# Optimization experiments

Hardware: AMD Instinct MI355X
Metric: run time of the kernel (lower is better)

The kernel has to match this reference:

```python
import math
import jax, jax.numpy as jnp
import numpy as np

B, H, S, D = 2, 16, 2048, 1024
DK = D // H  # 64


def setup_inputs() -> dict:
    key = jax.random.key(0)
    k1, k2, k3, k4, k5 = jax.random.split(key, 5)
    scale = np.float32(0.02)
    return {
        "x": jax.random.normal(k1, (B, H, S, D), dtype=jnp.float32),
        "wq": jax.random.normal(k2, (DK, D), dtype=jnp.float32) * scale,
        "wk": jax.random.normal(k3, (DK, D), dtype=jnp.float32) * scale,
        "wv": jax.random.normal(k4, (DK, D), dtype=jnp.float32) * scale,
        "wo": jax.random.normal(k5, (D, D), dtype=jnp.float32) * scale,
    }


def reference(x, wq, wk, wv, wo):
    # x: [B, H, S, D]; wq/wk/wv: [dk, D]; wo: [D, D]
    b, h, s, d = x.shape
    xq = jnp.einsum("bhsd,kd->bhsk", x, wq)  # [B,H,S,dk]
    xk = jnp.einsum("bhsd,kd->bhsk", x, wk)
    xv = jnp.einsum("bhsd,kd->bhsk", x, wv)
    # NOTE: original scales by sqrt(hidden_dim), not sqrt(dk)
    inv_scale = np.float32(1.0 / math.sqrt(d))
    score = jnp.einsum("bhsk,bhtk->bhst", xq, xk) * inv_scale  # [B,H,S,S]
    attn = jax.nn.softmax(score, axis=-1).astype(xq.dtype)
    out = jnp.einsum("bhst,bhtk->bhsk", attn, xv)  # [B,H,S,dk]
    out = out.transpose(0, 2, 1, 3).reshape(b, s, h * (wq.shape[0]))  # [B,S,H*dk]
    return out @ wo.T  # [B,S,D]
```

## Files before the change

### kernel.cpp

```cpp
#include <hip/hip_runtime.h>
#include <math.h>

#define BB 2
#define HH 16
#define SS 2048
#define DD 1024
#define DK 64
#define BHS (BB*HH*SS)
#define QSCALE 0.04508422f

typedef short  bf16x8  __attribute__((ext_vector_type(8)));
typedef float  floatx4 __attribute__((ext_vector_type(4)));
typedef unsigned short u16;

#define MFMA(a,b,c) __builtin_amdgcn_mfma_f32_16x16x32_bf16((a),(b),(c),0,0,0)

__device__ __forceinline__ unsigned cvt_pk_bf16(float lo, float hi) {
    unsigned r;
    asm("v_cvt_pk_bf16_f32 %0, %1, %2" : "=v"(r) : "v"(lo), "v"(hi));
    return r;
}
__device__ __forceinline__ bf16x8 ldfrag(const u16* p) {
    union { uint4 u; bf16x8 b; } c;
    c.u = *(const uint4*)p;
    return c.b;
}
__device__ __forceinline__ void stbf4(u16* p, float4 t) {
    union { unsigned u[2]; uint2 v; } c;
    c.u[0] = cvt_pk_bf16(t.x, t.y);
    c.u[1] = cvt_pk_bf16(t.z, t.w);
    *(uint2*)p = c.v;
}
__device__ __forceinline__ void st4s(u16* p, float a, float b, float c, float d) {
    unsigned x = cvt_pk_bf16(a, b), y = cvt_pk_bf16(c, d);
    p[0]  = (u16)x; p[16] = (u16)(x >> 16);
    p[32] = (u16)y; p[48] = (u16)(y >> 16);
}

#define WQKV_CHUNKS (192*1024/4)
#define WO_CHUNKS   (1024*1024/4)
__global__ __launch_bounds__(256) void convert_w(
    const float* __restrict__ wq, const float* __restrict__ wk,
    const float* __restrict__ wv, const float* __restrict__ wo,
    u16* __restrict__ wqkv, u16* __restrict__ wo_bf)
{
    int i = blockIdx.x * 256 + threadIdx.x;
    if (i < WQKV_CHUNKS) {
        int r = i >> 8;
        int c = i & 255;
        const float* src = (r < 64) ? wq : ((r < 128) ? wk : wv);
        float4 t = *(const float4*)(src + (size_t)(r & 63) * DD + c * 4);
        stbf4(wqkv + (size_t)r * DD + c * 4, t);
    } else if (i < WQKV_CHUNKS + WO_CHUNKS) {
        int j = i - WQKV_CHUNKS;
        float4 t = *(const float4*)(wo + (size_t)j * 4);
        stbf4(wo_bf + (size_t)j * 4, t);
    }
}

__global__ __launch_bounds__(256) void qkv_proj(
    const float* __restrict__ x, const u16* __restrict__ wqkv,
    u16* __restrict__ q, u16* __restrict__ k, u16* __restrict__ vT)
{
    __shared__ __align__(16) u16 Xs[64][72];
    __shared__ __align__(16) u16 Ws[192][72];
    const int tid  = threadIdx.x;
    const int w    = tid >> 6;
    const int lane = tid & 63;
    const int quad = lane >> 4;
    const int l16  = lane & 15;
    const int rowbase = blockIdx.x * 64;

    floatx4 acc[12];
#pragma unroll
    for (int n = 0; n < 12; ++n) acc[n] = (floatx4){0.f,0.f,0.f,0.f};

    for (int k0 = 0; k0 < DD; k0 += 64) {
#pragma unroll
        for (int it = 0; it < 4; ++it) {
            int li = tid + it * 256;
            int r  = li >> 4;
            int c4 = li & 15;
            float4 t = *(const float4*)(x + (size_t)(rowbase + r) * DD + k0 + c4 * 4);
            stbf4(&Xs[r][c4 * 4], t);
        }
#pragma unroll
        for (int it = 0; it < 6; ++it) {
            int li = tid + it * 256;
            int r  = li >> 3;
            int c8 = li & 7;
            *(uint4*)&Ws[r][c8 * 8] =
                *(const uint4*)(wqkv + (size_t)r * DD + k0 + c8 * 8);
        }
        __syncthreads();

        bf16x8 a0 = ldfrag(&Xs[w * 16 + l16][quad * 8]);
        bf16x8 a1 = ldfrag(&Xs[w * 16 + l16][32 + quad * 8]);
#pragma unroll
        for (int n = 0; n < 12; ++n) {
            bf16x8 b0 = ldfrag(&Ws[n * 16 + l16][quad * 8]);
            bf16x8 b1 = ldfrag(&Ws[n * 16 + l16][32 + quad * 8]);
            acc[n] = MFMA(a0, b0, acc[n]);
            acc[n] = MFMA(a1, b1, acc[n]);
        }
        __syncthreads();
    }

#pragma unroll
    for (int r = 0; r < 4; ++r) {
        int row = w * 16 + quad * 4 + r;
        size_t m = (size_t)(rowbase + row);
        st4s(&q[m * DK + l16], acc[0][r] * QSCALE, acc[1][r] * QSCALE,
                               acc[2][r] * QSCALE, acc[3][r] * QSCALE);
        st4s(&k[m * DK + l16], acc[4][r], acc[5][r], acc[6][r], acc[7][r]);
    }
    u16 (*Vbuf)[72] = Xs;
#pragma unroll
    for (int r = 0; r < 4; ++r) {
        int row = w * 16 + quad * 4 + r;
        st4s(&Vbuf[row][l16], acc[8][r], acc[9][r], acc[10][r], acc[11][r]);
    }
    __syncthreads();
    {
        const int dk = tid >> 2;
        const int sc = (tid & 3) * 16;
        const int bh = rowbase >> 11;
        const int s0 = rowbase & 2047;
        union { u16 s[16]; uint4 u[2]; } t;
#pragma unroll
        for (int u = 0; u < 16; ++u) t.s[u] = Vbuf[sc + u][dk];
        uint4* dst = (uint4*)(vT + ((size_t)(bh * DK + dk)) * SS + s0 + sc);
        dst[0] = t.u[0];
        dst[1] = t.u[1];
    }
}

__global__ __launch_bounds__(256) void flash_attn(
    const u16* __restrict__ q, const u16* __restrict__ k,
    const u16* __restrict__ vT, u16* __restrict__ ao)
{
    __shared__ __align__(16) u16 Qs[64][72];
    __shared__ __align__(16) u16 Ks[64][72];
    __shared__ __align__(16) u16 Vt[64][72];
    __shared__ __align__(16) u16 Ps[4][16][72];
    const int tid  = threadIdx.x;
    const int w    = tid >> 6;
    const int lane = tid & 63;
    const int quad = lane >> 4;
    const int l16  = lane & 15;
    const int qt   = blockIdx.x;
    const int bh   = blockIdx.y;
    const size_t kbase = (size_t)bh * SS * DK;
    const size_t vbase = (size_t)bh * DK * SS;

#pragma unroll
    for (int it = 0; it < 2; ++it) {
        int li = tid + it * 256;
        int r  = li >> 3;
        int c8 = li & 7;
        *(uint4*)&Qs[r][c8 * 8] =
            *(const uint4*)(q + kbase + (size_t)(qt * 64 + r) * DK + c8 * 8);
    }

    float m_i[4], l_i[4];
    floatx4 acc_o[4];
#pragma unroll
    for (int r = 0; r < 4; ++r) { m_i[r] = -INFINITY; l_i[r] = 0.f; }
#pragma unroll
    for (int n = 0; n < 4; ++n) acc_o[n] = (floatx4){0.f,0.f,0.f,0.f};
    __syncthreads();

    for (int kt = 0; kt < SS / 64; ++kt) {
#pragma unroll
        for (int it = 0; it < 2; ++it) {
            int li = tid + it * 256;
            int r  = li >> 3;
            int c8 = li & 7;
            *(uint4*)&Ks[r][c8 * 8] =
                *(const uint4*)(k + kbase + (size_t)(kt * 64 + r) * DK + c8 * 8);
            *(uint4*)&Vt[r][c8 * 8] =
                *(const uint4*)(vT + vbase + (size_t)r * SS + kt * 64 + c8 * 8);
        }
        __syncthreads();

        floatx4 sc[4];
        __builtin_amdgcn_s_setprio(1);
        {
            bf16x8 a0 = ldfrag(&Qs[w * 16 + l16][quad * 8]);
            bf16x8 a1 = ldfrag(&Qs[w * 16 + l16][32 + quad * 8]);
#pragma unroll
            for (int n = 0; n < 4; ++n) {
                sc[n] = (floatx4){0.f,0.f,0.f,0.f};
                bf16x8 b0 = ldfrag(&Ks[n * 16 + l16][quad * 8]);
                bf16x8 b1 = ldfrag(&Ks[n * 16 + l16][32 + quad * 8]);
                sc[n] = MFMA(a0, b0, sc[n]);
                sc[n] = MFMA(a1, b1, sc[n]);
            }
        }
        __builtin_amdgcn_s_setprio(0);

        float rmx[4];
#pragma unroll
        for (int r = 0; r < 4; ++r) {
            float rm = fmaxf(fmaxf(sc[0][r], sc[1][r]), fmaxf(sc[2][r], sc[3][r]));
#pragma unroll
            for (int off = 1; off < 16; off <<= 1)
                rm = fmaxf(rm, __shfl_xor(rm, off, 64));
            rmx[r] = rm;
        }
        int ok = (rmx[0] <= m_i[0] + 8.f) & (rmx[1] <= m_i[1] + 8.f) &
                 (rmx[2] <= m_i[2] + 8.f) & (rmx[3] <= m_i[3] + 8.f);
        if (!__all(ok)) {
#pragma unroll
            for (int r = 0; r < 4; ++r) {
                float mnew  = fmaxf(m_i[r], rmx[r]);
                float alpha = __builtin_amdgcn_exp2f(m_i[r] - mnew);
#pragma unroll
                for (int n = 0; n < 4; ++n) acc_o[n][r] *= alpha;
                l_i[r] *= alpha;
                m_i[r]  = mnew;
            }
        }
#pragma unroll
        for (int r = 0; r < 4; ++r) {
            float mi = m_i[r];
            float p0 = __builtin_amdgcn_exp2f(sc[0][r] - mi);
            float p1 = __builtin_amdgcn_exp2f(sc[1][r] - mi);
            float p2 = __builtin_amdgcn_exp2f(sc[2][r] - mi);
            float p3 = __builtin_amdgcn_exp2f(sc[3][r] - mi);
            float rs = (p0 + p1) + (p2 + p3);
#pragma unroll
            for (int off = 1; off < 16; off <<= 1)
                rs += __shfl_xor(rs, off, 64);
            l_i[r] += rs;
            st4s(&Ps[w][quad * 4 + r][l16], p0, p1, p2, p3);
        }

        __builtin_amdgcn_s_setprio(1);
#pragma unroll
        for (int kc = 0; kc < 2; ++kc) {
            bf16x8 a = ldfrag(&Ps[w][l16][kc * 32 + quad * 8]);
#pragma unroll
            for (int n = 0; n < 4; ++n) {
                bf16x8 b = ldfrag(&Vt[n * 16 + l16][kc * 32 + quad * 8]);
                acc_o[n] = MFMA(a, b, acc_o[n]);
            }
        }
        __builtin_amdgcn_s_setprio(0);
        __syncthreads();
    }

    const int b = bh >> 4, h = bh & 15;
#pragma unroll
    for (int r = 0; r < 4; ++r) {
        int srow = qt * 64 + w * 16 + quad * 4 + r;
        float rl = __builtin_amdgcn_rcpf(l_i[r]);
        size_t base = ((size_t)(b * SS + srow)) * (HH * DK) + h * 64;
        st4s(&ao[base + l16], acc_o[0][r] * rl, acc_o[1][r] * rl,
                              acc_o[2][r] * rl, acc_o[3][r] * rl);
    }
}

__global__ __launch_bounds__(256) void out_proj(
    const u16* __restrict__ ao, const u16* __restrict__ wo_bf,
    float* __restrict__ out)
{
    __shared__ __align__(16) u16 As[64][72];
    __shared__ __align__(16) u16 Bs[64][72];
    const int tid  = threadIdx.x;
    const int w    = tid >> 6;
    const int lane = tid & 63;
    const int quad = lane >> 4;
    const int l16  = lane & 15;
    const int mt = blockIdx.y;
    const int nt = blockIdx.x;

    floatx4 acc[4];
#pragma unroll
    for (int n = 0; n < 4; ++n) acc[n] = (floatx4){0.f,0.f,0.f,0.f};

    for (int k0 = 0; k0 < DD; k0 += 64) {
#pragma unroll
        for (int it = 0; it < 2; ++it) {
            int li = tid + it * 256;
            int r  = li >> 3;
            int c8 = li & 7;
            *(uint4*)&As[r][c8 * 8] =
                *(const uint4*)(ao + (size_t)(mt * 64 + r) * DD + k0 + c8 * 8);
            *(uint4*)&Bs[r][c8 * 8] =
                *(const uint4*)(wo_bf + (size_t)(nt * 64 + r) * DD + k0 + c8 * 8);
        }
        __syncthreads();

        bf16x8 a0 = ldfrag(&As[w * 16 + l16][quad * 8]);
        bf16x8 a1 = ldfrag(&As[w * 16 + l16][32 + quad * 8]);
#pragma unroll
        for (int n = 0; n < 4; ++n) {
            bf16x8 b0 = ldfrag(&Bs[n * 16 + l16][quad * 8]);
            bf16x8 b1 = ldfrag(&Bs[n * 16 + l16][32 + quad * 8]);
            acc[n] = MFMA(a0, b0, acc[n]);
            acc[n] = MFMA(a1, b1, acc[n]);
        }
        __syncthreads();
    }

#pragma unroll
    for (int r = 0; r < 4; ++r) {
        int row = mt * 64 + w * 16 + quad * 4 + r;
#pragma unroll
        for (int n = 0; n < 4; ++n)
            out[(size_t)row * DD + nt * 64 + n * 16 + l16] = acc[n][r];
    }
}

extern "C" void kernel_launch(void* const* d_in, const int* in_sizes, int n_in,
                              void* d_out, int out_size, void* d_ws, size_t ws_size,
                              hipStream_t stream) {
    const float* x  = (const float*)d_in[0];
    const float* wq = (const float*)d_in[1];
    const float* wk = (const float*)d_in[2];
    const float* wv = (const float*)d_in[3];
    const float* wo = (const float*)d_in[4];
    float* out = (float*)d_out;

    u16* q    = (u16*)d_ws;
    u16* k    = q    + (size_t)BHS * DK;
    u16* vT   = k    + (size_t)BHS * DK;
    u16* ao   = vT   + (size_t)BHS * DK;
    u16* wqkv = ao   + (size_t)BHS * DK;
    u16* wo_bf = wqkv + (size_t)192 * DD;

    convert_w<<<dim3((WQKV_CHUNKS + WO_CHUNKS) / 256), dim3(256), 0, stream>>>(
        wq, wk, wv, wo, wqkv, wo_bf);
    qkv_proj<<<dim3(BHS / 64), dim3(256), 0, stream>>>(x, wqkv, q, k, vT);
    flash_attn<<<dim3(SS / 64, BB * HH), dim3(256), 0, stream>>>(q, k, vT, ao);
    out_proj<<<dim3(DD / 64, (BB * SS) / 64), dim3(256), 0, stream>>>(ao, wo_bf, out);
}
```

Baseline: 574.6 us.

## Add register prefetch pipelining to all GEMM kernels and enlarge out_proj tiles

All three compute kernels now load the next K/V or weight tile into registers while computing on the current LDS tile, then store it to LDS between barriers, so global latency overlaps with MFMA work. qkv_proj moves to 512 threads split over row tiles and output-column groups, staging x in 256-wide chunks. out_proj grows from 64x64 to 128x128 tiles with 2x8 accumulators per wave for more operand reuse. The changes add register pressure and an extra barrier per iteration, and they set occupancy hints through launch_bounds.

After: 687.1 us. +19.6%, slower.

```diff
diff --git a/kernel.cpp b/kernel.cpp
--- a/kernel.cpp
+++ b/kernel.cpp
@@ -35,6 +35,10 @@
     unsigned x = cvt_pk_bf16(a, b), y = cvt_pk_bf16(c, d);
     p[0]  = (u16)x; p[16] = (u16)(x >> 16);
     p[32] = (u16)y; p[48] = (u16)(y >> 16);
+}
+__device__ __forceinline__ void st2s(u16* p, float a, float b) {
+    unsigned x = cvt_pk_bf16(a, b);
+    p[0]  = (u16)x; p[16] = (u16)(x >> 16);
 }
 
 #define WQKV_CHUNKS (192*1024/4)
@@ -58,84 +62,117 @@
     }
 }
 
-__global__ __launch_bounds__(256) void qkv_proj(
+__global__ __launch_bounds__(512, 4) void qkv_proj(
     const float* __restrict__ x, const u16* __restrict__ wqkv,
     u16* __restrict__ q, u16* __restrict__ k, u16* __restrict__ vT)
 {
-    __shared__ __align__(16) u16 Xs[64][72];
+    __shared__ __align__(16) u16 Xs[64][264];
     __shared__ __align__(16) u16 Ws[192][72];
     const int tid  = threadIdx.x;
     const int w    = tid >> 6;
     const int lane = tid & 63;
     const int quad = lane >> 4;
     const int l16  = lane & 15;
+    const int rt   = w & 3;
+    const int g    = w >> 2;
     const int rowbase = blockIdx.x * 64;
-
-    floatx4 acc[12];
-#pragma unroll
-    for (int n = 0; n < 12; ++n) acc[n] = (floatx4){0.f,0.f,0.f,0.f};
-
-    for (int k0 = 0; k0 < DD; k0 += 64) {
-#pragma unroll
-        for (int it = 0; it < 4; ++it) {
-            int li = tid + it * 256;
-            int r  = li >> 4;
-            int c4 = li & 15;
-            float4 t = *(const float4*)(x + (size_t)(rowbase + r) * DD + k0 + c4 * 4);
-            stbf4(&Xs[r][c4 * 4], t);
-        }
-#pragma unroll
-        for (int it = 0; it < 6; ++it) {
-            int li = tid + it * 256;
-            int r  = li >> 3;
-            int c8 = li & 7;
-            *(uint4*)&Ws[r][c8 * 8] =
-                *(const uint4*)(wqkv + (size_t)r * DD + k0 + c8 * 8);
-        }
-        __syncthreads();
-
-        bf16x8 a0 = ldfrag(&Xs[w * 16 + l16][quad * 8]);
-        bf16x8 a1 = ldfrag(&Xs[w * 16 + l16][32 + quad * 8]);
-#pragma unroll
-        for (int n = 0; n < 12; ++n) {
-            bf16x8 b0 = ldfrag(&Ws[n * 16 + l16][quad * 8]);
-            bf16x8 b1 = ldfrag(&Ws[n * 16 + l16][32 + quad * 8]);
-            acc[n] = MFMA(a0, b0, acc[n]);
-            acc[n] = MFMA(a1, b1, acc[n]);
-        }
-        __syncthreads();
-    }
-
-#pragma unroll
-    for (int r = 0; r < 4; ++r) {
-        int row = w * 16 + quad * 4 + r;
-        size_t m = (size_t)(rowbase + row);
-        st4s(&q[m * DK + l16], acc[0][r] * QSCALE, acc[1][r] * QSCALE,
-                               acc[2][r] * QSCALE, acc[3][r] * QSCALE);
-        st4s(&k[m * DK + l16], acc[4][r], acc[5][r], acc[6][r], acc[7][r]);
-    }
-    u16 (*Vbuf)[72] = Xs;
-#pragma unroll
-    for (int r = 0; r < 4; ++r) {
-        int row = w * 16 + quad * 4 + r;
-        st4s(&Vbuf[row][l16], acc[8][r], acc[9][r], acc[10][r], acc[11][r]);
+    const float* xb = x + (size_t)rowbase * DD;
+
+    float4 xreg[8];
+    uint4  wreg[3];
+
+    auto xload = [&](int qd) {
+#pragma unroll
+        for (int it = 0; it < 8; ++it) {
+            int li = tid + it * 512;
+            int r  = li >> 6, c4 = li & 63;
+            xreg[it] = *(const float4*)(xb + (size_t)r * DD + qd * 256 + c4 * 4);
+        }
+    };
+    auto xstore = [&]() {
+#pragma unroll
+        for (int it = 0; it < 8; ++it) {
+            int li = tid + it * 512;
+            int r  = li >> 6, c4 = li & 63;
+            stbf4(&Xs[r][c4 * 4], xreg[it]);
+        }
+    };
+    auto wload = [&](int kk) {
+#pragma unroll
+        for (int it = 0; it < 3; ++it) {
+            int li = tid + it * 512;
+            int r  = li >> 3, c8 = li & 7;
+            wreg[it] = *(const uint4*)(wqkv + (size_t)r * DD + kk * 64 + c8 * 8);
+        }
+    };
+    auto wstore = [&]() {
+#pragma unroll
+        for (int it = 0; it < 3; ++it) {
+            int li = tid + it * 512;
+            int r  = li >> 3, c8 = li & 7;
+            *(uint4*)&Ws[r][c8 * 8] = wreg[it];
+        }
+    };
+
+    floatx4 acc[6];
+#pragma unroll
+    for (int j = 0; j < 6; ++j) acc[j] = (floatx4){0.f,0.f,0.f,0.f};
+
+    xload(0); xstore();
+    wload(0); wstore();
+    __syncthreads();
+
+    for (int qd = 0; qd < 4; ++qd) {
+        if (qd < 3) xload(qd + 1);
+#pragma unroll
+        for (int ks = 0; ks < 4; ++ks) {
+            int kk = qd * 4 + ks;
+            if (kk < 15) wload(kk + 1);
+            bf16x8 a0 = ldfrag(&Xs[rt * 16 + l16][ks * 64 + quad * 8]);
+            bf16x8 a1 = ldfrag(&Xs[rt * 16 + l16][ks * 64 + 32 + quad * 8]);
+#pragma unroll
+            for (int j = 0; j < 6; ++j) {
+                int n = g * 6 + j;
+                bf16x8 b0 = ldfrag(&Ws[n * 16 + l16][quad * 8]);
+                bf16x8 b1 = ldfrag(&Ws[n * 16 + l16][32 + quad * 8]);
+                acc[j] = MFMA(a0, b0, acc[j]);
+                acc[j] = MFMA(a1, b1, acc[j]);
+            }
+            __syncthreads();
+            if (kk < 15) wstore();
+            if (ks == 3 && qd < 3) xstore();
+            __syncthreads();
+        }
+    }
+
+#pragma unroll
+    for (int rr = 0; rr < 4; ++rr) {
+        int rloc = rt * 16 + quad * 4 + rr;
+        size_t m = (size_t)(rowbase + rloc);
+        if (g == 0) {
+            st4s(&q[m * DK + l16], acc[0][rr] * QSCALE, acc[1][rr] * QSCALE,
+                                   acc[2][rr] * QSCALE, acc[3][rr] * QSCALE);
+            st2s(&k[m * DK + l16], acc[4][rr], acc[5][rr]);
+        } else {
+            st2s(&k[m * DK + 32 + l16], acc[0][rr], acc[1][rr]);
+            st4s(&Xs[rloc][l16], acc[2][rr], acc[3][rr],
+                                 acc[4][rr], acc[5][rr]);
+        }
     }
     __syncthreads();
     {
-        const int dk = tid >> 2;
-        const int sc = (tid & 3) * 16;
+        const int dk = tid >> 3;
+        const int sc = (tid & 7) * 8;
         const int bh = rowbase >> 11;
         const int s0 = rowbase & 2047;
-        union { u16 s[16]; uint4 u[2]; } t;
-#pragma unroll
-        for (int u = 0; u < 16; ++u) t.s[u] = Vbuf[sc + u][dk];
-        uint4* dst = (uint4*)(vT + ((size_t)(bh * DK + dk)) * SS + s0 + sc);
-        dst[0] = t.u[0];
-        dst[1] = t.u[1];
-    }
-}
-
-__global__ __launch_bounds__(256) void flash_attn(
+        union { u16 s[8]; uint4 u; } t;
+#pragma unroll
+        for (int u = 0; u < 8; ++u) t.s[u] = Xs[sc + u][dk];
+        *(uint4*)(vT + ((size_t)(bh * DK + dk)) * SS + s0 + sc) = t.u;
+    }
+}
+
+__global__ __launch_bounds__(256, 4) void flash_attn(
     const u16* __restrict__ q, const u16* __restrict__ k,
     const u16* __restrict__ vT, u16* __restrict__ ao)
 {
@@ -153,11 +190,30 @@
     const size_t kbase = (size_t)bh * SS * DK;
     const size_t vbase = (size_t)bh * DK * SS;
 
+    uint4 kreg[2], vreg[2];
+    auto kvload = [&](int kt) {
+#pragma unroll
+        for (int it = 0; it < 2; ++it) {
+            int li = tid + it * 256;
+            int r  = li >> 3, c8 = li & 7;
+            kreg[it] = *(const uint4*)(k + kbase + (size_t)(kt * 64 + r) * DK + c8 * 8);
+            vreg[it] = *(const uint4*)(vT + vbase + (size_t)r * SS + kt * 64 + c8 * 8);
+        }
+    };
+    auto kvstore = [&]() {
+#pragma unroll
+        for (int it = 0; it < 2; ++it) {
+            int li = tid + it * 256;
+            int r  = li >> 3, c8 = li & 7;
+            *(uint4*)&Ks[r][c8 * 8] = kreg[it];
+            *(uint4*)&Vt[r][c8 * 8] = vreg[it];
+        }
+    };
+
 #pragma unroll
     for (int it = 0; it < 2; ++it) {
         int li = tid + it * 256;
-        int r  = li >> 3;
-        int c8 = li & 7;
+        int r  = li >> 3, c8 = li & 7;
         *(uint4*)&Qs[r][c8 * 8] =
             *(const uint4*)(q + kbase + (size_t)(qt * 64 + r) * DK + c8 * 8);
     }
@@ -168,20 +224,12 @@
     for (int r = 0; r < 4; ++r) { m_i[r] = -INFINITY; l_i[r] = 0.f; }
 #pragma unroll
     for (int n = 0; n < 4; ++n) acc_o[n] = (floatx4){0.f,0.f,0.f,0.f};
+
+    kvload(0); kvstore();
     __syncthreads();
 
     for (int kt = 0; kt < SS / 64; ++kt) {
-#pragma unroll
-        for (int it = 0; it < 2; ++it) {
-            int li = tid + it * 256;
-            int r  = li >> 3;
-            int c8 = li & 7;
-            *(uint4*)&Ks[r][c8 * 8] =
-                *(const uint4*)(k + kbase + (size_t)(kt * 64 + r) * DK + c8 * 8);
-            *(uint4*)&Vt[r][c8 * 8] =
-                *(const uint4*)(vT + vbase + (size_t)r * SS + kt * 64 + c8 * 8);
-        }
-        __syncthreads();
+        if (kt < SS / 64 - 1) kvload(kt + 1);
 
         floatx4 sc[4];
         __builtin_amdgcn_s_setprio(1);
@@ -248,6 +296,8 @@
         }
         __builtin_amdgcn_s_setprio(0);
         __syncthreads();
+        if (kt < SS / 64 - 1) kvstore();
+        __syncthreads();
     }
 
     const int b = bh >> 4, h = bh & 15;
@@ -261,12 +311,12 @@
     }
 }
 
-__global__ __launch_bounds__(256) void out_proj(
+__global__ __launch_bounds__(256, 3) void out_proj(
     const u16* __restrict__ ao, const u16* __restrict__ wo_bf,
     float* __restrict__ out)
 {
-    __shared__ __align__(16) u16 As[64][72];
-    __shared__ __align__(16) u16 Bs[64][72];
+    __shared__ __align__(16) u16 As[128][72];
+    __shared__ __align__(16) u16 Bs[128][72];
     const int tid  = threadIdx.x;
     const int w    = tid >> 6;
     const int lane = tid & 63;
@@ -275,41 +325,62 @@
     const int mt = blockIdx.y;
     const int nt = blockIdx.x;
 
-    floatx4 acc[4];
-#pragma unroll
-    for (int n = 0; n < 4; ++n) acc[n] = (floatx4){0.f,0.f,0.f,0.f};
-
-    for (int k0 = 0; k0 < DD; k0 += 64) {
-#pragma unroll
-        for (int it = 0; it < 2; ++it) {
+    uint4 areg[4], breg[4];
+    auto abload = [&](int kk) {
+#pragma unroll
+        for (int it = 0; it < 4; ++it) {
             int li = tid + it * 256;
-            int r  = li >> 3;
-            int c8 = li & 7;
-            *(uint4*)&As[r][c8 * 8] =
-                *(const uint4*)(ao + (size_t)(mt * 64 + r) * DD + k0 + c8 * 8);
-            *(uint4*)&Bs[r][c8 * 8] =
-                *(const uint4*)(wo_bf + (size_t)(nt * 64 + r) * DD + k0 + c8 * 8);
+            int r  = li >> 3, c8 = li & 7;
+            areg[it] = *(const uint4*)(ao + (size_t)(mt * 128 + r) * DD + kk * 64 + c8 * 8);
+            breg[it] = *(const uint4*)(wo_bf + (size_t)(nt * 128 + r) * DD + kk * 64 + c8 * 8);
+        }
+    };
+    auto abstore = [&]() {
+#pragma unroll
+        for (int it = 0; it < 4; ++it) {
+            int li = tid + it * 256;
+            int r  = li >> 3, c8 = li & 7;
+            *(uint4*)&As[r][c8 * 8] = areg[it];
+            *(uint4*)&Bs[r][c8 * 8] = breg[it];
+        }
+    };
+
+    floatx4 acc[2][8];
+#pragma unroll
+    for (int rt = 0; rt < 2; ++rt)
+#pragma unroll
+        for (int n = 0; n < 8; ++n) acc[rt][n] = (floatx4){0.f,0.f,0.f,0.f};
+
+    abload(0); abstore();
+    __syncthreads();
+
+    for (int kk = 0; kk < 16; ++kk) {
+        if (kk < 15) abload(kk + 1);
+#pragma unroll
+        for (int kc = 0; kc < 2; ++kc) {
+            bf16x8 a0 = ldfrag(&As[w * 32 + l16][kc * 32 + quad * 8]);
+            bf16x8 a1 = ldfrag(&As[w * 32 + 16 + l16][kc * 32 + quad * 8]);
+#pragma unroll
+            for (int n = 0; n < 8; ++n) {
+                bf16x8 b = ldfrag(&Bs[n * 16 + l16][kc * 32 + quad * 8]);
+                acc[0][n] = MFMA(a0, b, acc[0][n]);
+                acc[1][n] = MFMA(a1, b, acc[1][n]);
+            }
         }
         __syncthreads();
-
-        bf16x8 a0 = ldfrag(&As[w * 16 + l16][quad * 8]);
-        bf16x8 a1 = ldfrag(&As[w * 16 + l16][32 + quad * 8]);
-#pragma unroll
-        for (int n = 0; n < 4; ++n) {
-            bf16x8 b0 = ldfrag(&Bs[n * 16 + l16][quad * 8]);
-            bf16x8 b1 = ldfrag(&Bs[n * 16 + l16][32 + quad * 8]);
-            acc[n] = MFMA(a0, b0, acc[n]);
-            acc[n] = MFMA(a1, b1, acc[n]);
-        }
+        if (kk < 15) abstore();
         __syncthreads();
     }
 
 #pragma unroll
-    for (int r = 0; r < 4; ++r) {
-        int row = mt * 64 + w * 16 + quad * 4 + r;
-#pragma unroll
-        for (int n = 0; n < 4; ++n)
-            out[(size_t)row * DD + nt * 64 + n * 16 + l16] = acc[n][r];
+    for (int rt = 0; rt < 2; ++rt) {
+#pragma unroll
+        for (int rr = 0; rr < 4; ++rr) {
+            int row = mt * 128 + w * 32 + rt * 16 + quad * 4 + rr;
+#pragma unroll
+            for (int n = 0; n < 8; ++n)
+                out[(size_t)row * DD + nt * 128 + n * 16 + l16] = acc[rt][n][rr];
+        }
     }
 }
 
@@ -323,16 +394,16 @@
     const float* wo = (const float*)d_in[4];
     float* out = (float*)d_out;
 
-    u16* q    = (u16*)d_ws;
-    u16* k    = q    + (size_t)BHS * DK;
-    u16* vT   = k    + (size_t)BHS * DK;
-    u16* ao   = vT   + (size_t)BHS * DK;
-    u16* wqkv = ao   + (size_t)BHS * DK;
+    u16* q     = (u16*)d_ws;
+    u16* k     = q    + (size_t)BHS * DK;
+    u16* vT    = k    + (size_t)BHS * DK;
+    u16* ao    = vT   + (size_t)BHS * DK;
+    u16* wqkv  = ao   + (size_t)BHS * DK;
     u16* wo_bf = wqkv + (size_t)192 * DD;
 
     convert_w<<<dim3((WQKV_CHUNKS + WO_CHUNKS) / 256), dim3(256), 0, stream>>>(
         wq, wk, wv, wo, wqkv, wo_bf);
-    qkv_proj<<<dim3(BHS / 64), dim3(256), 0, stream>>>(x, wqkv, q, k, vT);
+    qkv_proj<<<dim3(BHS / 64), dim3(512), 0, stream>>>(x, wqkv, q, k, vT);
     flash_attn<<<dim3(SS / 64, BB * HH), dim3(256), 0, stream>>>(q, k, vT, ao);
-    out_proj<<<dim3(DD / 64, (BB * SS) / 64), dim3(256), 0, stream>>>(ao, wo_bf, out);
-}
+    out_proj<<<dim3(DD / 128, (BB * SS) / 128), dim3(256), 0, stream>>>(ao, wo_bf, out);
+}
```
